# Performance work log

Hardware: AMD Instinct MI355X
Metric: run time of the kernel (lower is better)

## Reference

```python
import jax, jax.numpy as jnp
import numpy as np

N_NODES = 100000
N_EDGES = 1600000
D_IN = 128
D_HID = 128
D_OUT = 128


def setup_inputs() -> dict:
    key = jax.random.key(0)
    ks = jax.random.split(key, 8)
    x = jax.random.normal(ks[0], (N_NODES, D_IN), dtype=jnp.float32)
    edge_index = jax.random.randint(ks[1], (2, N_EDGES), 0, N_NODES, dtype=jnp.int32)
    s = 1.0 / np.sqrt(D_IN)
    # layer 0: D_IN -> D_HID ; layer 1: D_HID -> D_OUT
    W_l0 = jax.random.uniform(ks[2], (D_IN, D_HID), jnp.float32, -s, s)
    b_l0 = jnp.zeros((D_HID,), jnp.float32)
    W_r0 = jax.random.uniform(ks[3], (D_IN, D_HID), jnp.float32, -s, s)
    W_l1 = jax.random.uniform(ks[4], (D_HID, D_OUT), jnp.float32, -s, s)
    b_l1 = jnp.zeros((D_OUT,), jnp.float32)
    W_r1 = jax.random.uniform(ks[5], (D_HID, D_OUT), jnp.float32, -s, s)
    return {"x": x, "edge_index": edge_index,
            "W_l0": W_l0, "b_l0": b_l0, "W_r0": W_r0,
            "W_l1": W_l1, "b_l1": b_l1, "W_r1": W_r1}


def _sage_conv(x, src, dst, W_l, b_l, W_r):
    # PyG SAGEConv (aggr='mean'): out = lin_l(mean_{j in N(i)} x_j) + lin_r(x_i)
    msg = x[src]                                                  # [E, D] gather
    summed = jax.ops.segment_sum(msg, dst, num_segments=N_NODES)  # [N, D]
    cnt = jax.ops.segment_sum(jnp.ones((src.shape[0],), x.dtype), dst,
                              num_segments=N_NODES)               # [N]
    aggr = summed / jnp.maximum(cnt, 1.0)[:, None]                # mean; deg 0 -> 0
    return aggr @ W_l + b_l + x @ W_r


def reference(x, edge_index, W_l0, b_l0, W_r0, W_l1, b_l1, W_r1):
    src, dst = edge_index[0], edge_index[1]
    h = jax.nn.relu(_sage_conv(x, src, dst, W_l0, b_l0, W_r0))
    out = _sage_conv(h, src, dst, W_l1, b_l1, W_r1)
    return out
```

## Files before the change

### kernel.cpp

```cpp
#include <hip/hip_runtime.h>
#include <hip/hip_bf16.h>

#define N_NODES 100000
#define N_EDGES 1600000
#define D 128

typedef __attribute__((ext_vector_type(8))) short short8;
typedef __attribute__((ext_vector_type(4))) float f32x4;

__device__ __forceinline__ float bf2f(unsigned short u) {
    union { unsigned int i; float f; } c; c.i = ((unsigned int)u) << 16; return c.f;
}
__device__ __forceinline__ unsigned short f2bf(float f) {
    union { float f; unsigned int i; } c; c.f = f;
    unsigned int u = c.i;
    return (unsigned short)((u + 0x7fffu + ((u >> 16) & 1u)) >> 16);
}


__global__ __launch_bounds__(256) void k_pre(
    const int* __restrict__ dst, int* __restrict__ deg8, int* __restrict__ rank,
    const float* __restrict__ x, unsigned short* __restrict__ xb,
    const float* __restrict__ W0, const float* __restrict__ W1,
    const float* __restrict__ W2, const float* __restrict__ W3,
    unsigned short* __restrict__ T)
{
    int b = blockIdx.x;
    if (b < 6250) {
        int e = b * 256 + threadIdx.x;
        int c = b & 7;
        rank[e] = atomicAdd(&deg8[c * N_NODES + dst[e]], 1);
    } else if (b < 12500) {
        int i = (b - 6250) * 256 + threadIdx.x;
        int base = i * 8;
        float4 a = *(const float4*)&x[base];
        float4 v = *(const float4*)&x[base + 4];
        uint4 o;
        o.x = (unsigned)f2bf(a.x) | ((unsigned)f2bf(a.y) << 16);
        o.y = (unsigned)f2bf(a.z) | ((unsigned)f2bf(a.w) << 16);
        o.z = (unsigned)f2bf(v.x) | ((unsigned)f2bf(v.y) << 16);
        o.w = (unsigned)f2bf(v.z) | ((unsigned)f2bf(v.w) << 16);
        *(uint4*)&xb[base] = o;
    } else {
        int m = b - 12500;
        const float* W = (m == 0) ? W0 : (m == 1) ? W1 : (m == 2) ? W2 : W3;
        unsigned short* Tm = T + m * D * D;
        int n = threadIdx.x & 127;
        int kh = (threadIdx.x >> 7) * 64;
        for (int k = kh; k < kh + 64; ++k)
            Tm[n * D + k] = f2bf(W[k * D + n]);
    }
}

__global__ void k_scan1(const int* __restrict__ deg8, int* __restrict__ deg,
                        int* __restrict__ offsP, int* __restrict__ bsum) {
    __shared__ int s[256];
    int i = blockIdx.x * 256 + threadIdx.x;
    int v = 0;
    if (i < N_NODES) {
#pragma unroll
        for (int c = 0; c < 8; ++c) v += deg8[c * N_NODES + i];
        deg[i] = v;
    }
    s[threadIdx.x] = v;
    __syncthreads();
    for (int off = 1; off < 256; off <<= 1) {
        int t = (threadIdx.x >= off) ? s[threadIdx.x - off] : 0;
        __syncthreads();
        s[threadIdx.x] += t;
        __syncthreads();
    }
    if (i < N_NODES) offsP[i] = s[threadIdx.x] - v;
    if (threadIdx.x == 255) bsum[blockIdx.x] = s[255];
}

__global__ void k_scan2(int* __restrict__ bsum, int nb) {
    __shared__ int s[512];
    int t = threadIdx.x;
    int v = (t < nb) ? bsum[t] : 0;
    s[t] = v;
    __syncthreads();
    for (int off = 1; off < 512; off <<= 1) {
        int u = (t >= off) ? s[t - off] : 0;
        __syncthreads();
        s[t] += u;
        __syncthreads();
    }
    if (t < nb) bsum[t] = s[t] - v;
}

__global__ __launch_bounds__(256) void k_offs8(const int* __restrict__ offsP,
                                               const int* __restrict__ bsum,
                                               const int* __restrict__ deg8,
                                               int* __restrict__ offs,
                                               int* __restrict__ offs8) {
    int i = blockIdx.x * 256 + threadIdx.x;
    if (i < N_NODES) {
        int o = offsP[i] + bsum[blockIdx.x];
        offs[i] = o;
#pragma unroll
        for (int c = 0; c < 8; ++c) {
            offs8[c * N_NODES + i] = o;
            o += deg8[c * N_NODES + i];
        }
    }
}

__global__ __launch_bounds__(256) void k_place(const int* __restrict__ src,
                                               const int* __restrict__ dst,
                                               const int* __restrict__ rank,
                                               const int* __restrict__ offs8,
                                               int* __restrict__ csr) {
    int e = blockIdx.x * 256 + threadIdx.x;
    int c = blockIdx.x & 7;
    int d = dst[e];
    __builtin_nontemporal_store(src[e], &csr[offs8[c * N_NODES + d] + rank[e]]);
}


__global__ __launch_bounds__(256) void k_aggr_b(
    const unsigned short* __restrict__ xb, const int* __restrict__ offs,
    const int* __restrict__ deg, const int* __restrict__ csr,
    unsigned short* __restrict__ aggrb)
{
    int wave = threadIdx.x >> 6;
    int l = threadIdx.x & 63;
    int half = l >> 5;
    int li = l & 31;
    int node = blockIdx.x * 4 + wave;
    if (node >= N_NODES) return;
    int start = offs[node];
    int d = deg[node];
    float a0 = 0.f, a1 = 0.f, a2 = 0.f, a3 = 0.f;
    int e = 0;
    for (; e + 8 <= d; e += 8) {
        int j0 = csr[start + e + 0 + half];
        int j1 = csr[start + e + 2 + half];
        int j2 = csr[start + e + 4 + half];
        int j3 = csr[start + e + 6 + half];
        uint2 v0 = *(const uint2*)&xb[j0 * D + li * 4];
        uint2 v1 = *(const uint2*)&xb[j1 * D + li * 4];
        uint2 v2 = *(const uint2*)&xb[j2 * D + li * 4];
        uint2 v3 = *(const uint2*)&xb[j3 * D + li * 4];
        a0 += (bf2f(v0.x & 0xffff) + bf2f(v1.x & 0xffff)) + (bf2f(v2.x & 0xffff) + bf2f(v3.x & 0xffff));
        a1 += (bf2f(v0.x >> 16)    + bf2f(v1.x >> 16))    + (bf2f(v2.x >> 16)    + bf2f(v3.x >> 16));
        a2 += (bf2f(v0.y & 0xffff) + bf2f(v1.y & 0xffff)) + (bf2f(v2.y & 0xffff) + bf2f(v3.y & 0xffff));
        a3 += (bf2f(v0.y >> 16)    + bf2f(v1.y >> 16))    + (bf2f(v2.y >> 16)    + bf2f(v3.y >> 16));
    }
    for (; e + 2 <= d; e += 2) {
        int j = csr[start + e + half];
        uint2 v = *(const uint2*)&xb[j * D + li * 4];
        a0 += bf2f(v.x & 0xffff); a1 += bf2f(v.x >> 16);
        a2 += bf2f(v.y & 0xffff); a3 += bf2f(v.y >> 16);
    }
    if ((d & 1) && half == 0) {
        int j = csr[start + d - 1];
        uint2 v = *(const uint2*)&xb[j * D + li * 4];
        a0 += bf2f(v.x & 0xffff); a1 += bf2f(v.x >> 16);
        a2 += bf2f(v.y & 0xffff); a3 += bf2f(v.y >> 16);
    }
    a0 += __shfl_xor(a0, 32, 64);
    a1 += __shfl_xor(a1, 32, 64);
    a2 += __shfl_xor(a2, 32, 64);
    a3 += __shfl_xor(a3, 32, 64);
    if (half == 0) {
        float inv = 1.f / (float)(d > 0 ? d : 1);
        uint2 o;
        o.x = (unsigned)f2bf(a0 * inv) | ((unsigned)f2bf(a1 * inv) << 16);
        o.y = (unsigned)f2bf(a2 * inv) | ((unsigned)f2bf(a3 * inv) << 16);
        *(uint2*)&aggrb[node * D + li * 4] = o;
    }
}


template<int OUT_BF16, int RELU>
__global__ __launch_bounds__(256) void k_gemm_mfma(
    const unsigned short* __restrict__ Ab,
    const unsigned short* __restrict__ Bb,
    const unsigned short* __restrict__ Wlt,
    const unsigned short* __restrict__ Wrt,
    const float* __restrict__ bias,
    void* __restrict__ outp)
{
    __shared__ unsigned short As[128][40];
    __shared__ unsigned short Ws[128][40];

    int tid = threadIdx.x;
    int w = tid >> 6;
    int l = tid & 63;
    int row0 = blockIdx.x * 128;

    f32x4 acc[2][8];
#pragma unroll
    for (int h = 0; h < 2; ++h)
#pragma unroll
        for (int nt = 0; nt < 8; ++nt) acc[h][nt] = (f32x4){0.f, 0.f, 0.f, 0.f};

    for (int kt = 0; kt < 8; ++kt) {
        const unsigned short* Asrc = (kt < 4) ? Ab : Bb;
        const unsigned short* Wsrc = (kt < 4) ? Wlt : Wrt;
        int k0 = (kt & 3) * 32;
#pragma unroll
        for (int rep = 0; rep < 2; ++rep) {
            int idx = tid + 256 * rep;
            int rr = idx >> 2, c4 = idx & 3;
            int arow = row0 + rr; if (arow > N_NODES - 1) arow = N_NODES - 1;
            *(uint4*)&As[rr][c4 * 8] = *(const uint4*)&Asrc[arow * D + k0 + c4 * 8];
        }
#pragma unroll
        for (int rep = 0; rep < 2; ++rep) {
            int idx = tid + 256 * rep;
            int rr = idx >> 2, c4 = idx & 3;
            *(uint4*)&Ws[rr][c4 * 8] = *(const uint4*)&Wsrc[rr * D + k0 + c4 * 8];
        }
        __syncthreads();
        int kb = l >> 4, m16 = l & 15;
        short8 A0 = *(const short8*)&As[32 * w + m16][kb * 8];
        short8 A1 = *(const short8*)&As[32 * w + 16 + m16][kb * 8];
#pragma unroll
        for (int nt = 0; nt < 8; ++nt) {
            short8 b = *(const short8*)&Ws[nt * 16 + m16][kb * 8];
            acc[0][nt] = __builtin_amdgcn_mfma_f32_16x16x32_bf16(A0, b, acc[0][nt], 0, 0, 0);
            acc[1][nt] = __builtin_amdgcn_mfma_f32_16x16x32_bf16(A1, b, acc[1][nt], 0, 0, 0);
        }
        __syncthreads();
    }

    int cbase = l & 15;
#pragma unroll
    for (int h = 0; h < 2; ++h) {
        int rbase = row0 + 32 * w + 16 * h + ((l >> 4) << 2);
#pragma unroll
        for (int nt = 0; nt < 8; ++nt) {
            int col = nt * 16 + cbase;
            float bv = bias[col];
#pragma unroll
            for (int i = 0; i < 4; ++i) {
                int row = rbase + i;
                if (row < N_NODES) {
                    float v = acc[h][nt][i] + bv;
                    if (RELU) v = fmaxf(v, 0.f);
                    if (OUT_BF16) ((unsigned short*)outp)[row * D + col] = f2bf(v);
                    else          ((float*)outp)[row * D + col] = v;
                }
            }
        }
    }
}


static inline size_t align_up(size_t v, size_t a) { return (v + a - 1) / a * a; }

extern "C" void kernel_launch(void* const* d_in, const int* in_sizes, int n_in,
                              void* d_out, int out_size, void* d_ws, size_t ws_size,
                              hipStream_t stream) {
    const float* x   = (const float*)d_in[0];
    const int*   ei  = (const int*)d_in[1];
    const int*   src = ei;
    const int*   dst = ei + N_EDGES;
    const float* Wl0 = (const float*)d_in[2];
    const float* b0  = (const float*)d_in[3];
    const float* Wr0 = (const float*)d_in[4];
    const float* Wl1 = (const float*)d_in[5];
    const float* b1  = (const float*)d_in[6];
    const float* Wr1 = (const float*)d_in[7];
    float* out = (float*)d_out;

    char* w = (char*)d_ws;
    int* deg    = (int*)w;                  w += align_up(N_NODES * 4, 256);
    int* offs   = (int*)w;                  w += align_up(N_NODES * 4, 256);
    int* bsum   = (int*)w;                  w += align_up(512 * 4, 256);
    int* csr    = (int*)w;                  w += align_up((size_t)N_EDGES * 4, 256);
    unsigned short* xb    = (unsigned short*)w;  w += align_up((size_t)N_NODES * D * 2, 256);
    unsigned short* Wt    = (unsigned short*)w;  w += align_up((size_t)4 * D * D * 2, 256);
    unsigned short* aggrb = (unsigned short*)w;  w += align_up((size_t)N_NODES * D * 2, 256);
    int* deg8  = (int*)aggrb;
    int* rank  = deg8 + 8 * N_NODES;
    int* offs8 = rank + N_EDGES;
    unsigned short* Wt_l0 = Wt + 0 * D * D;
    unsigned short* Wt_r0 = Wt + 1 * D * D;
    unsigned short* Wt_l1 = Wt + 2 * D * D;
    unsigned short* Wt_r1 = Wt + 3 * D * D;

    const int nScanBlocks = (N_NODES + 255) / 256;
    const int nEdgeBlocks = N_EDGES / 256;
    const int nPreBlocks  = 6250 + 6250 + 4;
    const int nAggrBlocks = N_NODES / 4;
    const int nGemmBlocks = (N_NODES + 127) / 128;

    hipMemsetAsync(deg8, 0, (size_t)8 * N_NODES * sizeof(int), stream);
    k_pre<<<nPreBlocks, 256, 0, stream>>>(dst, deg8, rank, x, xb,
                                          Wl0, Wr0, Wl1, Wr1, Wt);
    k_scan1<<<nScanBlocks, 256, 0, stream>>>(deg8, deg, offs, bsum);
    k_scan2<<<1, 512, 0, stream>>>(bsum, nScanBlocks);
    k_offs8<<<nScanBlocks, 256, 0, stream>>>(offs, bsum, deg8, offs, offs8);
    k_place<<<nEdgeBlocks, 256, 0, stream>>>(src, dst, rank, offs8, csr);

    k_aggr_b<<<nAggrBlocks, 256, 0, stream>>>(xb, offs, deg, csr, aggrb);
    k_gemm_mfma<1, 1><<<nGemmBlocks, 256, 0, stream>>>(aggrb, xb, Wt_l0, Wt_r0, b0, xb);

    k_aggr_b<<<nAggrBlocks, 256, 0, stream>>>(xb, offs, deg, csr, aggrb);
    k_gemm_mfma<0, 0><<<nGemmBlocks, 256, 0, stream>>>(aggrb, xb, Wt_l1, Wt_r1, b1, out);
}
```

Before: 424.1 us.

## Widen aggregation gathers to 16B, redistribute preprocessing across kernels, drop nontemporal store

```diff
diff --git a/kernel.cpp b/kernel.cpp
--- a/kernel.cpp
+++ b/kernel.cpp
@@ -18,20 +18,21 @@
 }
 
 
-__global__ __launch_bounds__(256) void k_pre(
-    const int* __restrict__ dst, int* __restrict__ deg8, int* __restrict__ rank,
-    const float* __restrict__ x, unsigned short* __restrict__ xb,
-    const float* __restrict__ W0, const float* __restrict__ W1,
-    const float* __restrict__ W2, const float* __restrict__ W3,
-    unsigned short* __restrict__ T)
-{
+__global__ __launch_bounds__(256) void k_deg8(const int* __restrict__ dst,
+                                              int* __restrict__ deg8,
+                                              int* __restrict__ rank) {
+    int e = blockIdx.x * 256 + threadIdx.x;
+    int c = blockIdx.x & 7;
+    rank[e] = atomicAdd(&deg8[c * N_NODES + dst[e]], 1);
+}
+
+__global__ void k_scan1(const int* __restrict__ deg8, int* __restrict__ deg,
+                        int* __restrict__ offsP, int* __restrict__ bsum,
+                        const float* __restrict__ x, unsigned short* __restrict__ xb) {
+    __shared__ int s[256];
     int b = blockIdx.x;
-    if (b < 6250) {
-        int e = b * 256 + threadIdx.x;
-        int c = b & 7;
-        rank[e] = atomicAdd(&deg8[c * N_NODES + dst[e]], 1);
-    } else if (b < 12500) {
-        int i = (b - 6250) * 256 + threadIdx.x;
+    if (b >= 391) {
+        int i = (b - 391) * 256 + threadIdx.x;
         int base = i * 8;
         float4 a = *(const float4*)&x[base];
         float4 v = *(const float4*)&x[base + 4];
@@ -41,21 +42,9 @@
         o.z = (unsigned)f2bf(v.x) | ((unsigned)f2bf(v.y) << 16);
         o.w = (unsigned)f2bf(v.z) | ((unsigned)f2bf(v.w) << 16);
         *(uint4*)&xb[base] = o;
-    } else {
-        int m = b - 12500;
-        const float* W = (m == 0) ? W0 : (m == 1) ? W1 : (m == 2) ? W2 : W3;
-        unsigned short* Tm = T + m * D * D;
-        int n = threadIdx.x & 127;
-        int kh = (threadIdx.x >> 7) * 64;
-        for (int k = kh; k < kh + 64; ++k)
-            Tm[n * D + k] = f2bf(W[k * D + n]);
-    }
-}
-
-__global__ void k_scan1(const int* __restrict__ deg8, int* __restrict__ deg,
-                        int* __restrict__ offsP, int* __restrict__ bsum) {
-    __shared__ int s[256];
-    int i = blockIdx.x * 256 + threadIdx.x;
+        return;
+    }
+    int i = b * 256 + threadIdx.x;
     int v = 0;
     if (i < N_NODES) {
 #pragma unroll
@@ -71,7 +60,7 @@
         __syncthreads();
     }
     if (i < N_NODES) offsP[i] = s[threadIdx.x] - v;
-    if (threadIdx.x == 255) bsum[blockIdx.x] = s[255];
+    if (threadIdx.x == 255) bsum[b] = s[255];
 }
 
 __global__ void k_scan2(int* __restrict__ bsum, int nb) {
@@ -93,10 +82,26 @@
                                                const int* __restrict__ bsum,
                                                const int* __restrict__ deg8,
                                                int* __restrict__ offs,
-                                               int* __restrict__ offs8) {
-    int i = blockIdx.x * 256 + threadIdx.x;
+                                               int* __restrict__ offs8,
+                                               const float* __restrict__ W0,
+                                               const float* __restrict__ W1,
+                                               const float* __restrict__ W2,
+                                               const float* __restrict__ W3,
+                                               unsigned short* __restrict__ T) {
+    int b = blockIdx.x;
+    if (b >= 391) {
+        int m = b - 391;
+        const float* W = (m == 0) ? W0 : (m == 1) ? W1 : (m == 2) ? W2 : W3;
+        unsigned short* Tm = T + m * D * D;
+        int n = threadIdx.x & 127;
+        int kh = (threadIdx.x >> 7) * 64;
+        for (int k = kh; k < kh + 64; ++k)
+            Tm[n * D + k] = f2bf(W[k * D + n]);
+        return;
+    }
+    int i = b * 256 + threadIdx.x;
     if (i < N_NODES) {
-        int o = offsP[i] + bsum[blockIdx.x];
+        int o = offsP[i] + bsum[b];
         offs[i] = o;
 #pragma unroll
         for (int c = 0; c < 8; ++c) {
@@ -114,7 +119,7 @@
     int e = blockIdx.x * 256 + threadIdx.x;
     int c = blockIdx.x & 7;
     int d = dst[e];
-    __builtin_nontemporal_store(src[e], &csr[offs8[c * N_NODES + d] + rank[e]]);
+    csr[offs8[c * N_NODES + d] + rank[e]] = src[e];
 }
 
 
@@ -125,50 +130,62 @@
 {
     int wave = threadIdx.x >> 6;
     int l = threadIdx.x & 63;
-    int half = l >> 5;
-    int li = l & 31;
+    int g = l >> 4;
+    int li = l & 15;
     int node = blockIdx.x * 4 + wave;
     if (node >= N_NODES) return;
     int start = offs[node];
     int d = deg[node];
     float a0 = 0.f, a1 = 0.f, a2 = 0.f, a3 = 0.f;
+    float a4 = 0.f, a5 = 0.f, a6 = 0.f, a7 = 0.f;
     int e = 0;
     for (; e + 8 <= d; e += 8) {
-        int j0 = csr[start + e + 0 + half];
-        int j1 = csr[start + e + 2 + half];
-        int j2 = csr[start + e + 4 + half];
-        int j3 = csr[start + e + 6 + half];
-        uint2 v0 = *(const uint2*)&xb[j0 * D + li * 4];
-        uint2 v1 = *(const uint2*)&xb[j1 * D + li * 4];
-        uint2 v2 = *(const uint2*)&xb[j2 * D + li * 4];
-        uint2 v3 = *(const uint2*)&xb[j3 * D + li * 4];
-        a0 += (bf2f(v0.x & 0xffff) + bf2f(v1.x & 0xffff)) + (bf2f(v2.x & 0xffff) + bf2f(v3.x & 0xffff));
-        a1 += (bf2f(v0.x >> 16)    + bf2f(v1.x >> 16))    + (bf2f(v2.x >> 16)    + bf2f(v3.x >> 16));
-        a2 += (bf2f(v0.y & 0xffff) + bf2f(v1.y & 0xffff)) + (bf2f(v2.y & 0xffff) + bf2f(v3.y & 0xffff));
-        a3 += (bf2f(v0.y >> 16)    + bf2f(v1.y >> 16))    + (bf2f(v2.y >> 16)    + bf2f(v3.y >> 16));
-    }
-    for (; e + 2 <= d; e += 2) {
-        int j = csr[start + e + half];
-        uint2 v = *(const uint2*)&xb[j * D + li * 4];
+        int j0 = csr[start + e + g];
+        int j1 = csr[start + e + 4 + g];
+        uint4 v0 = *(const uint4*)&xb[j0 * D + li * 8];
+        uint4 v1 = *(const uint4*)&xb[j1 * D + li * 8];
+        a0 += bf2f(v0.x & 0xffff) + bf2f(v1.x & 0xffff);
+        a1 += bf2f(v0.x >> 16)    + bf2f(v1.x >> 16);
+        a2 += bf2f(v0.y & 0xffff) + bf2f(v1.y & 0xffff);
+        a3 += bf2f(v0.y >> 16)    + bf2f(v1.y >> 16);
+        a4 += bf2f(v0.z & 0xffff) + bf2f(v1.z & 0xffff);
+        a5 += bf2f(v0.z >> 16)    + bf2f(v1.z >> 16);
+        a6 += bf2f(v0.w & 0xffff) + bf2f(v1.w & 0xffff);
+        a7 += bf2f(v0.w >> 16)    + bf2f(v1.w >> 16);
+    }
+    if (e + 4 <= d) {
+        int j = csr[start + e + g];
+        uint4 v = *(const uint4*)&xb[j * D + li * 8];
         a0 += bf2f(v.x & 0xffff); a1 += bf2f(v.x >> 16);
         a2 += bf2f(v.y & 0xffff); a3 += bf2f(v.y >> 16);
-    }
-    if ((d & 1) && half == 0) {
-        int j = csr[start + d - 1];
-        uint2 v = *(const uint2*)&xb[j * D + li * 4];
+        a4 += bf2f(v.z & 0xffff); a5 += bf2f(v.z >> 16);
+        a6 += bf2f(v.w & 0xffff); a7 += bf2f(v.w >> 16);
+        e += 4;
+    }
+    if (e + g < d) {
+        int j = csr[start + e + g];
+        uint4 v = *(const uint4*)&xb[j * D + li * 8];
         a0 += bf2f(v.x & 0xffff); a1 += bf2f(v.x >> 16);
         a2 += bf2f(v.y & 0xffff); a3 += bf2f(v.y >> 16);
-    }
-    a0 += __shfl_xor(a0, 32, 64);
-    a1 += __shfl_xor(a1, 32, 64);
-    a2 += __shfl_xor(a2, 32, 64);
-    a3 += __shfl_xor(a3, 32, 64);
-    if (half == 0) {
+        a4 += bf2f(v.z & 0xffff); a5 += bf2f(v.z >> 16);
+        a6 += bf2f(v.w & 0xffff); a7 += bf2f(v.w >> 16);
+    }
+    a0 += __shfl_xor(a0, 16, 64); a0 += __shfl_xor(a0, 32, 64);
+    a1 += __shfl_xor(a1, 16, 64); a1 += __shfl_xor(a1, 32, 64);
+    a2 += __shfl_xor(a2, 16, 64); a2 += __shfl_xor(a2, 32, 64);
+    a3 += __shfl_xor(a3, 16, 64); a3 += __shfl_xor(a3, 32, 64);
+    a4 += __shfl_xor(a4, 16, 64); a4 += __shfl_xor(a4, 32, 64);
+    a5 += __shfl_xor(a5, 16, 64); a5 += __shfl_xor(a5, 32, 64);
+    a6 += __shfl_xor(a6, 16, 64); a6 += __shfl_xor(a6, 32, 64);
+    a7 += __shfl_xor(a7, 16, 64); a7 += __shfl_xor(a7, 32, 64);
+    if (g == 0) {
         float inv = 1.f / (float)(d > 0 ? d : 1);
-        uint2 o;
+        uint4 o;
         o.x = (unsigned)f2bf(a0 * inv) | ((unsigned)f2bf(a1 * inv) << 16);
         o.y = (unsigned)f2bf(a2 * inv) | ((unsigned)f2bf(a3 * inv) << 16);
-        *(uint2*)&aggrb[node * D + li * 4] = o;
+        o.z = (unsigned)f2bf(a4 * inv) | ((unsigned)f2bf(a5 * inv) << 16);
+        o.w = (unsigned)f2bf(a6 * inv) | ((unsigned)f2bf(a7 * inv) << 16);
+        *(uint4*)&aggrb[node * D + li * 8] = o;
     }
 }
 
@@ -284,16 +301,15 @@
 
     const int nScanBlocks = (N_NODES + 255) / 256;
     const int nEdgeBlocks = N_EDGES / 256;
-    const int nPreBlocks  = 6250 + 6250 + 4;
     const int nAggrBlocks = N_NODES / 4;
     const int nGemmBlocks = (N_NODES + 127) / 128;
 
     hipMemsetAsync(deg8, 0, (size_t)8 * N_NODES * sizeof(int), stream);
-    k_pre<<<nPreBlocks, 256, 0, stream>>>(dst, deg8, rank, x, xb,
-                                          Wl0, Wr0, Wl1, Wr1, Wt);
-    k_scan1<<<nScanBlocks, 256, 0, stream>>>(deg8, deg, offs, bsum);
+    k_deg8<<<nEdgeBlocks, 256, 0, stream>>>(dst, deg8, rank);
+    k_scan1<<<nScanBlocks + 6250, 256, 0, stream>>>(deg8, deg, offs, bsum, x, xb);
     k_scan2<<<1, 512, 0, stream>>>(bsum, nScanBlocks);
-    k_offs8<<<nScanBlocks, 256, 0, stream>>>(offs, bsum, deg8, offs, offs8);
+    k_offs8<<<nScanBlocks + 4, 256, 0, stream>>>(offs, bsum, deg8, offs, offs8,
+                                                 Wl0, Wr0, Wl1, Wr1, Wt);
     k_place<<<nEdgeBlocks, 256, 0, stream>>>(src, dst, rank, offs8, csr);
 
     k_aggr_b<<<nAggrBlocks, 256, 0, stream>>>(xb, offs, deg, csr, aggrb);
```

Result: faster. 410.5 us (-3.2%).
